# Optimization experiments

Measured on AMD Instinct MI355X. Metric: run time of the kernel, lower is better.

Reference implementation:

```python
import jax, jax.numpy as jnp
import numpy as np

N_NODES = 50000
N_EDGES = 600000
N_GRAPHS = 256


def gcn_conv(x, W, b, src, dst, n):
    # PyG GCNConv: out = D^{-1/2} (A + I) D^{-1/2} X W + b
    h = x @ W  # [N, out]
    deg = jax.ops.segment_sum(jnp.ones((src.shape[0],), h.dtype), dst, num_segments=n) + 1.0  # self-loop
    dinv = jax.lax.rsqrt(deg)  # deg >= 1 so safe
    msgs = h[src] * (dinv[src] * dinv[dst])[:, None]  # [E, out]
    agg = jax.ops.segment_sum(msgs, dst, num_segments=n)
    agg = agg + h * (dinv * dinv)[:, None]  # self-loop contribution
    return agg + b


def setup_inputs() -> dict:
    key = jax.random.key(0)
    ks = jax.random.split(key, 8)
    x = jax.random.normal(ks[0], (N_NODES, 1), dtype=jnp.float32)
    edge_index = jax.random.randint(ks[1], (2, N_EDGES), 0, N_NODES, dtype=jnp.int64)
    batch = jnp.sort(jax.random.randint(ks[2], (N_NODES,), 0, N_GRAPHS, dtype=jnp.int64))

    def glorot(k, shape):
        lim = np.sqrt(6.0 / (shape[0] + shape[1]))
        return jax.random.uniform(k, shape, jnp.float32, -lim, lim)

    return {
        "x": x,
        "W1": glorot(ks[3], (1, 64)), "b1": jnp.zeros((64,), jnp.float32),
        "W2": glorot(ks[4], (64, 128)), "b2": jnp.zeros((128,), jnp.float32),
        "W3": glorot(ks[5], (128, 64)), "b3": jnp.zeros((64,), jnp.float32),
        "lin1_w": glorot(ks[6], (64, 32)), "lin1_b": jnp.zeros((32,), jnp.float32),
        "lin2_w": glorot(ks[7], (32, 1)), "lin2_b": jnp.zeros((1,), jnp.float32),
        "edge_index": edge_index,
        "batch": batch,
    }


def reference(x, W1, b1, W2, b2, W3, b3, lin1_w, lin1_b, lin2_w, lin2_b, edge_index, batch):
    src, dst = edge_index[0], edge_index[1]
    n = x.shape[0]
    h = jax.nn.relu(gcn_conv(x, W1, b1, src, dst, n))
    h = jax.nn.relu(gcn_conv(h, W2, b2, src, dst, n))
    h = jax.nn.relu(gcn_conv(h, W3, b3, src, dst, n))
    # global_mean_pool
    sums = jax.ops.segment_sum(h, batch, num_segments=N_GRAPHS)
    cnts = jax.ops.segment_sum(jnp.ones((n,), h.dtype), batch, num_segments=N_GRAPHS)
    pooled = sums / jnp.maximum(cnts, 1.0)[:, None]  # [G, 64]
    z = jax.nn.relu(pooled @ lin1_w + lin1_b)
    return z @ lin2_w + lin2_b  # [G, 1]
```

## Files before the change

### kernel.cpp

```cpp
#include <hip/hip_runtime.h>
#include <hip/hip_fp16.h>


#define N_FEAT 64
#define POOL_SUB 16
#define SLOT 64

typedef _Float16 f16x4 __attribute__((ext_vector_type(4)));
typedef float f32x4 __attribute__((ext_vector_type(4)));

__global__ void fill_kernel(const int* __restrict__ src, const int* __restrict__ dst,
                            int* __restrict__ deg, int* __restrict__ csr, int E) {
    int e4 = (blockIdx.x * blockDim.x + threadIdx.x) * 4;
    if (e4 + 3 < E) {
        int4 sv = *(const int4*)&src[e4];
        int4 dv = *(const int4*)&dst[e4];
        int p0 = atomicAdd(&deg[dv.x], 1);
        int p1 = atomicAdd(&deg[dv.y], 1);
        int p2 = atomicAdd(&deg[dv.z], 1);
        int p3 = atomicAdd(&deg[dv.w], 1);
        csr[dv.x * SLOT + p0] = sv.x;
        csr[dv.y * SLOT + p1] = sv.y;
        csr[dv.z * SLOT + p2] = sv.z;
        csr[dv.w * SLOT + p3] = sv.w;
    } else {
        for (int e = e4; e < E; ++e) {
            int d = dst[e];
            int pos = atomicAdd(&deg[d], 1);
            csr[d * SLOT + pos] = src[e];
        }
    }
}

__global__ void prep_kernel(const int* __restrict__ deg, const float* __restrict__ x,
                            float* __restrict__ dinv, float* __restrict__ xd,
                            const float* __restrict__ W2, const float* __restrict__ W3,
                            __half* __restrict__ W2p, __half* __restrict__ W3p, int N) {
    int i = blockIdx.x * blockDim.x + threadIdx.x;
    if (i < N) {
        float dv = rsqrtf((float)deg[i] + 1.0f);
        dinv[i] = dv;
        xd[i] = x[i] * dv;
    }
    if (i < 16384) {
        if (i < 8192) {
            int ii = i & 3;
            int lane = (i >> 2) & 63;
            int blk = i >> 8;
            int k = (blk & 3) * 16 + (lane >> 4) * 4 + ii;
            int col = (blk >> 2) * 16 + (lane & 15);
            W2p[i] = __float2half(W2[k * 128 + col]);
        } else {
            int t2 = i - 8192;
            int ii = t2 & 3;
            int lane = (t2 >> 2) & 63;
            int blk = t2 >> 8;
            int k = (blk & 7) * 16 + (lane >> 4) * 4 + ii;
            int col = (blk >> 3) * 16 + (lane & 15);
            W3p[t2] = __float2half(W3[k * 64 + col]);
        }
    }
}

__global__ void sagg_gather(const int* __restrict__ deg, const int* __restrict__ csr,
                            const float* __restrict__ xd, const float* __restrict__ dinv,
                            float2* __restrict__ sd, int N) {
    int wid = (blockIdx.x * blockDim.x + threadIdx.x) >> 6;
    int lane = threadIdx.x & 63;
    int v = wid * 4 + (lane >> 4);
    int sub = lane & 15;
    if (v >= N) return;
    int dg = deg[v];
    int base = v * SLOT;
    float sum = 0.0f;
    for (int j = sub; j < dg; j += 16) sum += xd[csr[base + j]];
    #pragma unroll
    for (int off = 8; off; off >>= 1) sum += __shfl_xor(sum, off);
    if (sub == 0) {
        float dv = dinv[v];
        sd[v] = make_float2(dv * (sum + xd[v]), dv);
    }
}

__global__ void agg1_gather(const int* __restrict__ deg, const int* __restrict__ csr,
                            const float2* __restrict__ sd,
                            const float* __restrict__ W1, const float* __restrict__ b1,
                            __half* __restrict__ agg16, int N) {
    int wave = (blockIdx.x * blockDim.x + threadIdx.x) >> 6;
    int lane = threadIdx.x & 63;
    int v = wave * 2 + (lane >> 5);
    int sub = lane & 31;
    if (v >= N) return;
    float2 w  = *(const float2*)&W1[sub * 2];
    float2 bb = *(const float2*)&b1[sub * 2];
    int dg = deg[v];
    int base = v * SLOT;
    float ax = 0.0f, ay = 0.0f;
    int j = 0;
    for (; j + 3 < dg; j += 4) {
        int4 u = *(const int4*)&csr[base + j];
        float2 p0 = sd[u.x];
        float2 p1 = sd[u.y];
        float2 p2 = sd[u.z];
        float2 p3 = sd[u.w];
        ax += fmaxf(p0.x * w.x + bb.x, 0.0f) * p0.y + fmaxf(p1.x * w.x + bb.x, 0.0f) * p1.y;
        ax += fmaxf(p2.x * w.x + bb.x, 0.0f) * p2.y + fmaxf(p3.x * w.x + bb.x, 0.0f) * p3.y;
        ay += fmaxf(p0.x * w.y + bb.y, 0.0f) * p0.y + fmaxf(p1.x * w.y + bb.y, 0.0f) * p1.y;
        ay += fmaxf(p2.x * w.y + bb.y, 0.0f) * p2.y + fmaxf(p3.x * w.y + bb.y, 0.0f) * p3.y;
    }
    for (; j < dg; ++j) {
        float2 p = sd[csr[base + j]];
        ax += fmaxf(p.x * w.x + bb.x, 0.0f) * p.y;
        ay += fmaxf(p.x * w.y + bb.y, 0.0f) * p.y;
    }
    float2 pv = sd[v];
    float dv = pv.y;
    float ox = dv * ax + fmaxf(pv.x * w.x + bb.x, 0.0f) * dv * dv;
    float oy = dv * ay + fmaxf(pv.x * w.y + bb.y, 0.0f) * dv * dv;
    *(__half2*)&agg16[(size_t)v * N_FEAT + sub * 2] = __floats2half2_rn(ox, oy);
}

#define H2PAD 136
__global__ __launch_bounds__(256) void gemm12(const __half* __restrict__ A16,
                                              const __half* __restrict__ W2p,
                                              const float* __restrict__ bias2,
                                              const __half* __restrict__ W3p,
                                              const float* __restrict__ dinv,
                                              __half* __restrict__ md, int M) {
    __shared__ __half h2s[32 * H2PAD];
    int tid = threadIdx.x;
    int wave = tid >> 6, lane = tid & 63;
    int g = lane >> 4, r = lane & 15;
    int row0 = blockIdx.x * 32;

    f16x4 af[2][4];
    #pragma unroll
    for (int rt = 0; rt < 2; ++rt) {
        int row = row0 + rt * 16 + r;
        if (row >= M) row = M - 1;
        const __half* ap = A16 + (size_t)row * 64 + g * 4;
        #pragma unroll
        for (int kc = 0; kc < 4; ++kc)
            af[rt][kc] = *(const f16x4*)(ap + kc * 16);
    }

    f32x4 acc[2][2] = {};
    const f16x4* w2v = (const f16x4*)W2p;
    #pragma unroll
    for (int ctl = 0; ctl < 2; ++ctl) {
        int ct = wave * 2 + ctl;
        #pragma unroll
        for (int kc = 0; kc < 4; ++kc) {
            f16x4 bf = w2v[(ct * 4 + kc) * 64 + lane];
            acc[0][ctl] = __builtin_amdgcn_mfma_f32_16x16x16f16(af[0][kc], bf, acc[0][ctl], 0, 0, 0);
            acc[1][ctl] = __builtin_amdgcn_mfma_f32_16x16x16f16(af[1][kc], bf, acc[1][ctl], 0, 0, 0);
        }
    }
    #pragma unroll
    for (int ctl = 0; ctl < 2; ++ctl) {
        int col = (wave * 2 + ctl) * 16 + r;
        float bb = bias2[col];
        #pragma unroll
        for (int rt = 0; rt < 2; ++rt)
            #pragma unroll
            for (int i = 0; i < 4; ++i)
                h2s[(rt * 16 + g * 4 + i) * H2PAD + col] =
                    __float2half(fmaxf(acc[rt][ctl][i] + bb, 0.f));
    }
    __syncthreads();

    f32x4 acc2[2] = {};
    const f16x4* w3v = (const f16x4*)W3p;
    #pragma unroll
    for (int kc = 0; kc < 8; ++kc) {
        f16x4 bf = w3v[(wave * 8 + kc) * 64 + lane];
        #pragma unroll
        for (int rt = 0; rt < 2; ++rt) {
            f16x4 a2 = *(const f16x4*)&h2s[(rt * 16 + r) * H2PAD + kc * 16 + g * 4];
            acc2[rt] = __builtin_amdgcn_mfma_f32_16x16x16f16(a2, bf, acc2[rt], 0, 0, 0);
        }
    }
    #pragma unroll
    for (int rt = 0; rt < 2; ++rt)
        #pragma unroll
        for (int i = 0; i < 4; ++i) {
            int row = row0 + rt * 16 + g * 4 + i;
            if (row < M)
                md[(size_t)row * 64 + wave * 16 + r] = __float2half(acc2[rt][i] * dinv[row]);
        }
}

__global__ void agg3_gather(const int* __restrict__ deg, const int* __restrict__ csr,
                            const __half* __restrict__ md, const float* __restrict__ dinv,
                            float* __restrict__ agg, int N) {
    int wave = (blockIdx.x * blockDim.x + threadIdx.x) >> 6;
    int lane = threadIdx.x & 63;
    int v = wave * 8 + (lane >> 3);
    int sub = lane & 7;
    if (v >= N) return;
    const uint4* mdp = (const uint4*)md;
    int dg = deg[v];
    int base = v * SLOT;
    float a0, a1, a2, a3, a4, a5, a6, a7;
    {
        uint4 sv = mdp[(size_t)v * 8 + sub];
        float2 f0 = __half22float2(*(const __half2*)&sv.x);
        float2 f1 = __half22float2(*(const __half2*)&sv.y);
        float2 f2 = __half22float2(*(const __half2*)&sv.z);
        float2 f3 = __half22float2(*(const __half2*)&sv.w);
        a0 = f0.x; a1 = f0.y; a2 = f1.x; a3 = f1.y;
        a4 = f2.x; a5 = f2.y; a6 = f3.x; a7 = f3.y;
    }
    int j = 0;
    for (; j + 3 < dg; j += 4) {
        int4 u = *(const int4*)&csr[base + j];
        uint4 x0 = mdp[(size_t)u.x * 8 + sub];
        uint4 x1 = mdp[(size_t)u.y * 8 + sub];
        uint4 x2 = mdp[(size_t)u.z * 8 + sub];
        uint4 x3 = mdp[(size_t)u.w * 8 + sub];
        #define ACC8(X) { \
            float2 t0 = __half22float2(*(const __half2*)&X.x); \
            float2 t1 = __half22float2(*(const __half2*)&X.y); \
            float2 t2 = __half22float2(*(const __half2*)&X.z); \
            float2 t3 = __half22float2(*(const __half2*)&X.w); \
            a0 += t0.x; a1 += t0.y; a2 += t1.x; a3 += t1.y;    \
            a4 += t2.x; a5 += t2.y; a6 += t3.x; a7 += t3.y; }
        ACC8(x0) ACC8(x1) ACC8(x2) ACC8(x3)
    }
    for (; j < dg; ++j) {
        uint4 xv = mdp[(size_t)csr[base + j] * 8 + sub];
        ACC8(xv)
        #undef ACC8
    }
    float dv = dinv[v];
    float* op = &agg[(size_t)v * N_FEAT + sub * 8];
    *(float4*)op       = make_float4(a0 * dv, a1 * dv, a2 * dv, a3 * dv);
    *(float4*)(op + 4) = make_float4(a4 * dv, a5 * dv, a6 * dv, a7 * dv);
}

__global__ void pool_kernel(const float* __restrict__ agg, const float* __restrict__ b3,
                            const int* __restrict__ batch, float* __restrict__ pooled,
                            float* __restrict__ counts, int N) {
    int wave = (blockIdx.x * blockDim.x + threadIdx.x) >> 6;
    int lane = threadIdx.x & 63;
    int start = wave * POOL_SUB;
    if (start >= N) return;
    int end = min(start + POOL_SUB, N);
    float bl = b3[lane];
    int cur = batch[start];
    float acc = 0.0f;
    float cnt = 0.0f;
    for (int i = start; i < end; ++i) {
        int g = batch[i];
        if (g != cur) {
            atomicAdd(&pooled[cur * N_FEAT + lane], acc);
            if (lane == 0) atomicAdd(&counts[cur], cnt);
            acc = 0.0f; cnt = 0.0f; cur = g;
        }
        acc += fmaxf(agg[(size_t)i * N_FEAT + lane] + bl, 0.0f);
        cnt += 1.0f;
    }
    atomicAdd(&pooled[cur * N_FEAT + lane], acc);
    if (lane == 0) atomicAdd(&counts[cur], cnt);
}

__global__ void mlp_kernel(const float* __restrict__ pooled, const float* __restrict__ counts,
                           const float* __restrict__ l1w, const float* __restrict__ l1b,
                           const float* __restrict__ l2w, const float* __restrict__ l2b,
                           float* __restrict__ out) {
    __shared__ float row[64];
    __shared__ float zs[32];
    int g = blockIdx.x;
    int l = threadIdx.x;
    float cnt = fmaxf(counts[g], 1.0f);
    row[l] = pooled[g * 64 + l] / cnt;
    __syncthreads();
    if (l < 32) {
        float z = l1b[l];
        #pragma unroll
        for (int k = 0; k < 64; ++k) z += row[k] * l1w[k * 32 + l];
        zs[l] = fmaxf(z, 0.0f);
    }
    __syncthreads();
    if (l == 0) {
        float o = l2b[0];
        #pragma unroll
        for (int j = 0; j < 32; ++j) o += zs[j] * l2w[j];
        out[g] = o;
    }
}

extern "C" void kernel_launch(void* const* d_in, const int* in_sizes, int n_in,
                              void* d_out, int out_size, void* d_ws, size_t ws_size,
                              hipStream_t stream) {
    const float* x   = (const float*)d_in[0];
    const float* W1  = (const float*)d_in[1];
    const float* b1  = (const float*)d_in[2];
    const float* W2  = (const float*)d_in[3];
    const float* b2  = (const float*)d_in[4];
    const float* W3  = (const float*)d_in[5];
    const float* b3  = (const float*)d_in[6];
    const float* l1w = (const float*)d_in[7];
    const float* l1b = (const float*)d_in[8];
    const float* l2w = (const float*)d_in[9];
    const float* l2b = (const float*)d_in[10];
    const int* ei    = (const int*)d_in[11];
    const int* batch = (const int*)d_in[12];

    int N = in_sizes[0];
    int E = in_sizes[11] / 2;
    int G = out_size;
    const int* src = ei;
    const int* dst = ei + E;

    char* wsb = (char*)d_ws;
    int*   deg      = (int*)wsb;                 wsb += (size_t)N * 4;
    float* pooled   = (float*)wsb;               wsb += (size_t)G * 64 * 4;
    float* counts   = (float*)wsb;               wsb += (size_t)G * 4;
    int*   csr      = (int*)wsb;                 wsb += (size_t)N * SLOT * 4;
    float* dinv     = (float*)wsb;               wsb += (size_t)N * 4;
    float* xd       = (float*)wsb;               wsb += (size_t)N * 4;
    float2* sd      = (float2*)wsb;              wsb += (size_t)N * 8;
    float* agg      = (float*)wsb;               wsb += (size_t)N * 64 * 4;
    __half* md      = (__half*)wsb;              wsb += (size_t)N * 64 * 2;
    __half* agg16   = (__half*)wsb;              wsb += ((size_t)N + 32) * 64 * 2;
    __half* W2p     = (__half*)wsb;              wsb += 8192 * 2;
    __half* W3p     = (__half*)wsb;              wsb += 8192 * 2;

    hipMemsetAsync(deg, 0, ((size_t)N + (size_t)G * 64 + G) * 4, stream);

    int tb = 256;
    fill_kernel<<<(E / 4 + tb - 1) / tb, tb, 0, stream>>>(src, dst, deg, csr, E);
    prep_kernel<<<(N + tb - 1) / tb, tb, 0, stream>>>(deg, x, dinv, xd, W2, W3, W2p, W3p, N);
    sagg_gather<<<((N + 3) / 4 + 3) / 4, tb, 0, stream>>>(deg, csr, xd, dinv, sd, N);
    int a1_waves = (N + 1) / 2;
    agg1_gather<<<(a1_waves + 3) / 4, tb, 0, stream>>>(deg, csr, sd, W1, b1, agg16, N);
    gemm12<<<(N + 31) / 32, tb, 0, stream>>>(agg16, W2p, b2, W3p, dinv, md, N);
    int a3_waves = (N + 7) / 8;
    agg3_gather<<<(a3_waves + 3) / 4, tb, 0, stream>>>(deg, csr, md, dinv, agg, N);
    int pool_waves = (N + POOL_SUB - 1) / POOL_SUB;
    pool_kernel<<<(pool_waves + 3) / 4, tb, 0, stream>>>(agg, b3, batch, pooled, counts, N);
    mlp_kernel<<<G, 64, 0, stream>>>(pooled, counts, l1w, l1b, l2w, l2b, (float*)d_out);
}
```

Baseline: 192.8 us.

## Split layer-3 features into two 32-wide halves and store aggregation in fp16

The gemm output is written as two separate 32-column fp16 arrays, and the layer-3 gather runs twice, once per half. Each half-array is 3.2 MB instead of 6.4 MB, so the random neighbor gathers are meant to hit the cache more often. The aggregated output is also stored in fp16 instead of fp32, which halves the bytes pool_kernel reads. This adds a kernel launch, rereads the CSR indices twice, and loses some precision in the stored aggregation.

```diff
diff --git a/kernel.cpp b/kernel.cpp
--- a/kernel.cpp
+++ b/kernel.cpp
@@ -126,7 +126,8 @@
                                               const float* __restrict__ bias2,
                                               const __half* __restrict__ W3p,
                                               const float* __restrict__ dinv,
-                                              __half* __restrict__ md, int M) {
+                                              __half* __restrict__ mdA,
+                                              __half* __restrict__ mdB, int M) {
     __shared__ __half h2s[32 * H2PAD];
     int tid = threadIdx.x;
     int wave = tid >> 6, lane = tid & 63;
@@ -180,30 +181,32 @@
             acc2[rt] = __builtin_amdgcn_mfma_f32_16x16x16f16(a2, bf, acc2[rt], 0, 0, 0);
         }
     }
+    __half* mdx = (wave < 2) ? mdA : mdB;
+    int colx = (wave & 1) * 16 + r;
     #pragma unroll
     for (int rt = 0; rt < 2; ++rt)
         #pragma unroll
         for (int i = 0; i < 4; ++i) {
             int row = row0 + rt * 16 + g * 4 + i;
             if (row < M)
-                md[(size_t)row * 64 + wave * 16 + r] = __float2half(acc2[rt][i] * dinv[row]);
+                mdx[(size_t)row * 32 + colx] = __float2half(acc2[rt][i] * dinv[row]);
         }
 }
 
 __global__ void agg3_gather(const int* __restrict__ deg, const int* __restrict__ csr,
-                            const __half* __restrict__ md, const float* __restrict__ dinv,
-                            float* __restrict__ agg, int N) {
+                            const __half* __restrict__ mdh, const float* __restrict__ dinv,
+                            __half* __restrict__ aggh, int N) {
     int wave = (blockIdx.x * blockDim.x + threadIdx.x) >> 6;
     int lane = threadIdx.x & 63;
-    int v = wave * 8 + (lane >> 3);
-    int sub = lane & 7;
+    int v = wave * 16 + (lane >> 2);
+    int sub = lane & 3;
     if (v >= N) return;
-    const uint4* mdp = (const uint4*)md;
+    const uint4* mdp = (const uint4*)mdh;
     int dg = deg[v];
     int base = v * SLOT;
     float a0, a1, a2, a3, a4, a5, a6, a7;
     {
-        uint4 sv = mdp[(size_t)v * 8 + sub];
+        uint4 sv = mdp[(size_t)v * 4 + sub];
         float2 f0 = __half22float2(*(const __half2*)&sv.x);
         float2 f1 = __half22float2(*(const __half2*)&sv.y);
         float2 f2 = __half22float2(*(const __half2*)&sv.z);
@@ -214,10 +217,10 @@
     int j = 0;
     for (; j + 3 < dg; j += 4) {
         int4 u = *(const int4*)&csr[base + j];
-        uint4 x0 = mdp[(size_t)u.x * 8 + sub];
-        uint4 x1 = mdp[(size_t)u.y * 8 + sub];
-        uint4 x2 = mdp[(size_t)u.z * 8 + sub];
-        uint4 x3 = mdp[(size_t)u.w * 8 + sub];
+        uint4 x0 = mdp[(size_t)u.x * 4 + sub];
+        uint4 x1 = mdp[(size_t)u.y * 4 + sub];
+        uint4 x2 = mdp[(size_t)u.z * 4 + sub];
+        uint4 x3 = mdp[(size_t)u.w * 4 + sub];
         #define ACC8(X) { \
             float2 t0 = __half22float2(*(const __half2*)&X.x); \
             float2 t1 = __half22float2(*(const __half2*)&X.y); \
@@ -228,24 +231,28 @@
         ACC8(x0) ACC8(x1) ACC8(x2) ACC8(x3)
     }
     for (; j < dg; ++j) {
-        uint4 xv = mdp[(size_t)csr[base + j] * 8 + sub];
+        uint4 xv = mdp[(size_t)csr[base + j] * 4 + sub];
         ACC8(xv)
         #undef ACC8
     }
     float dv = dinv[v];
-    float* op = &agg[(size_t)v * N_FEAT + sub * 8];
-    *(float4*)op       = make_float4(a0 * dv, a1 * dv, a2 * dv, a3 * dv);
-    *(float4*)(op + 4) = make_float4(a4 * dv, a5 * dv, a6 * dv, a7 * dv);
-}
-
-__global__ void pool_kernel(const float* __restrict__ agg, const float* __restrict__ b3,
-                            const int* __restrict__ batch, float* __restrict__ pooled,
-                            float* __restrict__ counts, int N) {
+    __half2* op = (__half2*)&aggh[(size_t)v * 32 + sub * 8];
+    op[0] = __floats2half2_rn(a0 * dv, a1 * dv);
+    op[1] = __floats2half2_rn(a2 * dv, a3 * dv);
+    op[2] = __floats2half2_rn(a4 * dv, a5 * dv);
+    op[3] = __floats2half2_rn(a6 * dv, a7 * dv);
+}
+
+__global__ void pool_kernel(const __half* __restrict__ aggA, const __half* __restrict__ aggB,
+                            const float* __restrict__ b3, const int* __restrict__ batch,
+                            float* __restrict__ pooled, float* __restrict__ counts, int N) {
     int wave = (blockIdx.x * blockDim.x + threadIdx.x) >> 6;
     int lane = threadIdx.x & 63;
     int start = wave * POOL_SUB;
     if (start >= N) return;
     int end = min(start + POOL_SUB, N);
+    const __half* basep = (lane < 32) ? aggA : aggB;
+    int f = lane & 31;
     float bl = b3[lane];
     int cur = batch[start];
     float acc = 0.0f;
@@ -257,7 +264,7 @@
             if (lane == 0) atomicAdd(&counts[cur], cnt);
             acc = 0.0f; cnt = 0.0f; cur = g;
         }
-        acc += fmaxf(agg[(size_t)i * N_FEAT + lane] + bl, 0.0f);
+        acc += fmaxf(__half2float(basep[(size_t)i * 32 + f]) + bl, 0.0f);
         cnt += 1.0f;
     }
     atomicAdd(&pooled[cur * N_FEAT + lane], acc);
@@ -321,8 +328,10 @@
     float* dinv     = (float*)wsb;               wsb += (size_t)N * 4;
     float* xd       = (float*)wsb;               wsb += (size_t)N * 4;
     float2* sd      = (float2*)wsb;              wsb += (size_t)N * 8;
-    float* agg      = (float*)wsb;               wsb += (size_t)N * 64 * 4;
-    __half* md      = (__half*)wsb;              wsb += (size_t)N * 64 * 2;
+    __half* mdA     = (__half*)wsb;              wsb += (size_t)N * 32 * 2;
+    __half* mdB     = (__half*)wsb;              wsb += (size_t)N * 32 * 2;
+    __half* aggA    = (__half*)wsb;              wsb += (size_t)N * 32 * 2;
+    __half* aggB    = (__half*)wsb;              wsb += (size_t)N * 32 * 2;
     __half* agg16   = (__half*)wsb;              wsb += ((size_t)N + 32) * 64 * 2;
     __half* W2p     = (__half*)wsb;              wsb += 8192 * 2;
     __half* W3p     = (__half*)wsb;              wsb += 8192 * 2;
@@ -335,10 +344,12 @@
     sagg_gather<<<((N + 3) / 4 + 3) / 4, tb, 0, stream>>>(deg, csr, xd, dinv, sd, N);
     int a1_waves = (N + 1) / 2;
     agg1_gather<<<(a1_waves + 3) / 4, tb, 0, stream>>>(deg, csr, sd, W1, b1, agg16, N);
-    gemm12<<<(N + 31) / 32, tb, 0, stream>>>(agg16, W2p, b2, W3p, dinv, md, N);
-    int a3_waves = (N + 7) / 8;
-    agg3_gather<<<(a3_waves + 3) / 4, tb, 0, stream>>>(deg, csr, md, dinv, agg, N);
+    gemm12<<<(N + 31) / 32, tb, 0, stream>>>(agg16, W2p, b2, W3p, dinv, mdA, mdB, N);
+    int a3_waves = (N + 15) / 16;
+    int a3_blocks = (a3_waves + 3) / 4;
+    agg3_gather<<<a3_blocks, tb, 0, stream>>>(deg, csr, mdA, dinv, aggA, N);
+    agg3_gather<<<a3_blocks, tb, 0, stream>>>(deg, csr, mdB, dinv, aggB, N);
     int pool_waves = (N + POOL_SUB - 1) / POOL_SUB;
-    pool_kernel<<<(pool_waves + 3) / 4, tb, 0, stream>>>(agg, b3, batch, pooled, counts, N);
+    pool_kernel<<<(pool_waves + 3) / 4, tb, 0, stream>>>(aggA, aggB, b3, batch, pooled, counts, N);
     mlp_kernel<<<G, 64, 0, stream>>>(pooled, counts, l1w, l1b, l2w, l2b, (float*)d_out);
 }
```

After: 193.6 us. No clear change (+0.4%).
